# Optimization experiments

Hardware: AMD Instinct MI355X
Metric: run time of the kernel (lower is better)

## Reference

```python
import jax, jax.numpy as jnp
import numpy as np

NUM_HEADS = 16
HIDDEN = 1024
MASKED_BIAS = -10000.0


def setup_inputs() -> dict:
    key = jax.random.key(0)
    k1, k2 = jax.random.split(key)
    encodings = jax.random.normal(k1, (4, 2048, HIDDEN), dtype=jnp.float32)
    W_attn = jax.random.normal(k2, (HIDDEN, 3 * HIDDEN), dtype=jnp.float32) * (HIDDEN ** -0.5)
    b_attn = jnp.zeros((3 * HIDDEN,), dtype=jnp.float32)
    return {"encodings": encodings, "W_attn": W_attn, "b_attn": b_attn}


def reference(encodings, W_attn, b_attn):
    b, s, hidden = encodings.shape
    head_size = hidden // NUM_HEADS
    cattn = encodings @ W_attn + b_attn  # [b, s, 3*hidden]
    q, k, v = jnp.split(cattn, 3, axis=-1)
    # [b, s, hidden] -> [b, h, s, c]
    def split_heads(x):
        return x.reshape(b, s, NUM_HEADS, head_size).transpose(0, 2, 1, 3)
    q, k, v = split_heads(q), split_heads(k), split_heads(v)
    scores = jnp.einsum('bhfc,bhtc->bhft', q, k) / np.sqrt(head_size).astype(np.float32)
    causal = jnp.tril(jnp.ones((s, s), dtype=bool))[None, None]
    scores = jnp.where(causal, scores, jnp.float32(MASKED_BIAS))
    patterns = jax.nn.softmax(scores, axis=-1)
    ctx = jnp.einsum('bhft,bhtc->bhfc', patterns, v)
    # [b, h, s, c] -> [b, s, hidden]
    return ctx.transpose(0, 2, 1, 3).reshape(b, s, hidden)
```

## Files before the change

### kernel.cpp

```cpp
#include <hip/hip_runtime.h>

#define B_   4
#define S_   2048
#define HID  1024
#define NH   16
#define CH   64
#define M_   (B_ * S_)
#define N3   (3 * HID)
#define LDT2 72

typedef __attribute__((ext_vector_type(4))) float f32x4;
typedef __attribute__((ext_vector_type(8))) unsigned short u16x8;
typedef __attribute__((ext_vector_type(4))) unsigned short u16x4;

__device__ __forceinline__ unsigned short f2bf(float x) {
    unsigned u = __builtin_bit_cast(unsigned, x);
    u += 0x7fffu + ((u >> 16) & 1u);
    return (unsigned short)(u >> 16);
}
__device__ __forceinline__ float bf2f(unsigned short h) {
    unsigned u = ((unsigned)h) << 16;
    return __builtin_bit_cast(float, u);
}
__device__ __forceinline__ f32x4 mfma16(u16x8 a, u16x8 b, f32x4 c) {
    asm("v_mfma_f32_16x16x32_bf16 %0, %1, %2, %0" : "+v"(c) : "v"(a), "v"(b));
    return c;
}

__global__ __launch_bounds__(256) void k_split(const float* __restrict__ x,
                                               unsigned short* __restrict__ hi,
                                               unsigned short* __restrict__ lo,
                                               int n8) {
    int idx = blockIdx.x * 256 + threadIdx.x;
    if (idx >= n8) return;
    const f32x4* px = (const f32x4*)x + (size_t)idx * 2;
    f32x4 a = px[0], b = px[1];
    u16x8 h, l;
#pragma unroll
    for (int i = 0; i < 8; i++) {
        float xv = (i < 4) ? a[i] : b[i - 4];
        unsigned short hb = f2bf(xv);
        h[i] = hb;
        l[i] = f2bf(xv - bf2f(hb));
    }
    *(u16x8*)(hi + (size_t)idx * 8) = h;
    *(u16x8*)(lo + (size_t)idx * 8) = l;
}

__global__ __launch_bounds__(256) void k_tsplit(const float* __restrict__ W,
                                                unsigned short* __restrict__ WTh,
                                                unsigned short* __restrict__ WTl) {
    __shared__ float tile[32][33];
    int n0 = blockIdx.x * 32, k0 = blockIdx.y * 32;
    int tid = threadIdx.x;
    int r = tid >> 3, c0 = (tid & 7) * 4;
    f32x4 v = *(const f32x4*)(W + (size_t)(k0 + r) * N3 + n0 + c0);
#pragma unroll
    for (int i = 0; i < 4; i++) tile[r][c0 + i] = v[i];
    __syncthreads();
    u16x4 h, l;
#pragma unroll
    for (int i = 0; i < 4; i++) {
        float xv = tile[c0 + i][r];
        unsigned short hb = f2bf(xv);
        h[i] = hb;
        l[i] = f2bf(xv - bf2f(hb));
    }
    size_t o = (size_t)(n0 + r) * HID + k0 + c0;
    *(u16x4*)(WTh + o) = h;
    *(u16x4*)(WTl + o) = l;
}

__global__ __launch_bounds__(256, 2) void k_gemm(
    const unsigned short* __restrict__ Ah, const unsigned short* __restrict__ Al,
    const unsigned short* __restrict__ Bh, const unsigned short* __restrict__ Bl,
    const float* __restrict__ bias,
    unsigned short* __restrict__ Qh, unsigned short* __restrict__ Ql,
    unsigned short* __restrict__ Kh, unsigned short* __restrict__ Kl,
    unsigned short* __restrict__ Vt) {
    __shared__ __attribute__((aligned(16))) unsigned short sAh[128 * LDT2];
    __shared__ __attribute__((aligned(16))) unsigned short sAl[128 * LDT2];
    __shared__ __attribute__((aligned(16))) unsigned short sBh[128 * LDT2];
    __shared__ __attribute__((aligned(16))) unsigned short sBl[128 * LDT2];
    int tid = threadIdx.x;
    int m0 = blockIdx.y * 128, n0 = blockIdx.x * 128;
    int r = tid >> 1, kh2 = (tid & 1) * 32;
    int lane = tid & 63, w = tid >> 6;
    int wm = (w >> 1) * 64, wn = (w & 1) * 64;
    int l15 = lane & 15, l4 = lane >> 4;
    f32x4 acc[4][4] = {};
    size_t gA = (size_t)(m0 + r) * HID + kh2;
    size_t gB = (size_t)(n0 + r) * HID + kh2;

    u16x8 pf[4][4];
#pragma unroll
    for (int j = 0; j < 4; j++) {
        pf[0][j] = *(const u16x8*)(Ah + gA + j * 8);
        pf[1][j] = *(const u16x8*)(Al + gA + j * 8);
        pf[2][j] = *(const u16x8*)(Bh + gB + j * 8);
        pf[3][j] = *(const u16x8*)(Bl + gB + j * 8);
    }
#pragma unroll
    for (int j = 0; j < 4; j++) {
        *(u16x8*)&sAh[r * LDT2 + kh2 + j * 8] = pf[0][j];
        *(u16x8*)&sAl[r * LDT2 + kh2 + j * 8] = pf[1][j];
        *(u16x8*)&sBh[r * LDT2 + kh2 + j * 8] = pf[2][j];
        *(u16x8*)&sBl[r * LDT2 + kh2 + j * 8] = pf[3][j];
    }

    for (int k0 = 0; k0 < HID; k0 += 64) {
        __syncthreads();
        bool more = (k0 + 64 < HID);
        if (more) {
#pragma unroll
            for (int j = 0; j < 4; j++) {
                pf[0][j] = *(const u16x8*)(Ah + gA + k0 + 64 + j * 8);
                pf[1][j] = *(const u16x8*)(Al + gA + k0 + 64 + j * 8);
                pf[2][j] = *(const u16x8*)(Bh + gB + k0 + 64 + j * 8);
                pf[3][j] = *(const u16x8*)(Bl + gB + k0 + 64 + j * 8);
            }
        }
#pragma unroll
        for (int ks = 0; ks < 64; ks += 32) {
            u16x8 a0[4], a1[4], b0[4], b1[4];
#pragma unroll
            for (int i = 0; i < 4; i++) {
                int off = ks + l4 * 8;
                int row = wm + i * 16 + l15;
                a0[i] = *(const u16x8*)&sAh[row * LDT2 + off];
                a1[i] = *(const u16x8*)&sAl[row * LDT2 + off];
                int rowb = wn + i * 16 + l15;
                b0[i] = *(const u16x8*)&sBh[rowb * LDT2 + off];
                b1[i] = *(const u16x8*)&sBl[rowb * LDT2 + off];
            }
#pragma unroll
            for (int mt = 0; mt < 4; mt++)
#pragma unroll
                for (int nt = 0; nt < 4; nt++) {
                    acc[mt][nt] = mfma16(a0[mt], b0[nt], acc[mt][nt]);
                    acc[mt][nt] = mfma16(a0[mt], b1[nt], acc[mt][nt]);
                    acc[mt][nt] = mfma16(a1[mt], b0[nt], acc[mt][nt]);
                }
        }
        __syncthreads();
        if (more) {
#pragma unroll
            for (int j = 0; j < 4; j++) {
                *(u16x8*)&sAh[r * LDT2 + kh2 + j * 8] = pf[0][j];
                *(u16x8*)&sAl[r * LDT2 + kh2 + j * 8] = pf[1][j];
                *(u16x8*)&sBh[r * LDT2 + kh2 + j * 8] = pf[2][j];
                *(u16x8*)&sBl[r * LDT2 + kh2 + j * 8] = pf[3][j];
            }
        }
    }

#pragma unroll
    for (int mt = 0; mt < 4; mt++)
#pragma unroll
        for (int nt = 0; nt < 4; nt++) {
            int n = n0 + wn + nt * 16 + l15;
            float bv = bias[n];
            int which = n >> 10, hid = n & 1023;
            int h = hid >> 6, c = hid & 63;
            int mbase = m0 + wm + mt * 16 + l4 * 4;
            int b = mbase >> 11, sbase = mbase & 2047;
            int bh = b * NH + h;
            if (which == 2) {
                u16x4 pv;
#pragma unroll
                for (int jj = 0; jj < 4; jj++) pv[jj] = f2bf(acc[mt][nt][jj] + bv);
                *(u16x4*)(Vt + ((size_t)bh * CH + c) * S_ + sbase) = pv;
            } else {
                unsigned short* __restrict__ dh = (which == 0) ? Qh : Kh;
                unsigned short* __restrict__ dl = (which == 0) ? Ql : Kl;
                float sc = (which == 0) ? 0.125f : 1.0f;
#pragma unroll
                for (int jj = 0; jj < 4; jj++) {
                    float val = (acc[mt][nt][jj] + bv) * sc;
                    unsigned short hb = f2bf(val);
                    size_t so = ((size_t)bh * S_ + sbase + jj) * CH + c;
                    dh[so] = hb;
                    dl[so] = f2bf(val - bf2f(hb));
                }
            }
        }
}

__global__ __launch_bounds__(256, 2) void k_attn(const unsigned short* __restrict__ Qh,
                                                 const unsigned short* __restrict__ Ql,
                                                 const unsigned short* __restrict__ Kh,
                                                 const unsigned short* __restrict__ Kl,
                                                 const unsigned short* __restrict__ Vt,
                                                 float* __restrict__ out) {
    __shared__ __attribute__((aligned(16))) unsigned short sKh[128 * 64];
    __shared__ __attribute__((aligned(16))) unsigned short sKl[128 * 64];
    __shared__ __attribute__((aligned(16))) unsigned short sVT[64 * 128];
    __shared__ __attribute__((aligned(16))) unsigned short sP[4][32 * 128];
    int tid = threadIdx.x, lane = tid & 63, w = tid >> 6;
    int l15 = lane & 15, l4 = lane >> 4;
    int qt = gridDim.x - 1 - blockIdx.x;
    int bh = blockIdx.y;
    int b = bh >> 4, h = bh & 15;
    size_t head_off = (size_t)bh * S_ * CH;
    const unsigned short* Qhp = Qh + head_off;
    const unsigned short* Qlp = Ql + head_off;
    const unsigned short* Khp = Kh + head_off;
    const unsigned short* Klp = Kl + head_off;
    const unsigned short* Vtp = Vt + (size_t)bh * CH * S_;

    u16x8 qh[2][2], ql[2][2];
#pragma unroll
    for (int m = 0; m < 2; m++)
#pragma unroll
        for (int cc = 0; cc < 2; cc++) {
            size_t o = (size_t)(qt * 128 + w * 32 + m * 16 + l15) * CH + cc * 32 + l4 * 8;
            qh[m][cc] = *(const u16x8*)(Qhp + o);
            ql[m][cc] = *(const u16x8*)(Qlp + o);
        }

    f32x4 ctx[2][4] = {};
    float mrun[2][4], lrun[2][4];
#pragma unroll
    for (int m = 0; m < 2; m++)
#pragma unroll
        for (int j = 0; j < 4; j++) { mrun[m][j] = -1e30f; lrun[m][j] = 0.f; }

    for (int kt = 0; kt <= qt; kt++) {
        __syncthreads();
#pragma unroll
        for (int j = 0; j < 4; j++) {
            int idx = tid + j * 256;
            int rr = idx >> 3, slot = idx & 7;
            size_t g = (size_t)(kt * 128 + rr) * CH + slot * 8;
            int bo = (slot * 16) ^ ((rr & 7) << 4);
            *(u16x8*)((char*)sKh + rr * 128 + bo) = *(const u16x8*)(Khp + g);
            *(u16x8*)((char*)sKl + rr * 128 + bo) = *(const u16x8*)(Klp + g);
        }
#pragma unroll
        for (int j = 0; j < 4; j++) {
            int idx = tid + j * 256;
            int cc = idx >> 4, slot = idx & 15;
            size_t g = (size_t)cc * S_ + kt * 128 + slot * 8;
            int bo = (slot * 16) ^ ((cc & 7) << 4);
            *(u16x8*)((char*)sVT + cc * 256 + bo) = *(const u16x8*)(Vtp + g);
        }
        __syncthreads();

        f32x4 sa[2][8];
#pragma unroll
        for (int m = 0; m < 2; m++)
#pragma unroll
            for (int nt = 0; nt < 8; nt++) sa[m][nt] = f32x4{0.f, 0.f, 0.f, 0.f};
#pragma unroll
        for (int nt = 0; nt < 8; nt++) {
            int rowb = nt * 16 + l15;
            int swb = (rowb & 7) << 4;
            u16x8 kbh[2], kbl[2];
#pragma unroll
            for (int cc = 0; cc < 2; cc++) {
                int off = (cc * 64 + l4 * 16) ^ swb;
                kbh[cc] = *(const u16x8*)((char*)sKh + rowb * 128 + off);
                kbl[cc] = *(const u16x8*)((char*)sKl + rowb * 128 + off);
            }
#pragma unroll
            for (int m = 0; m < 2; m++)
#pragma unroll
                for (int cc = 0; cc < 2; cc++) {
                    sa[m][nt] = mfma16(qh[m][cc], kbh[cc], sa[m][nt]);
                    sa[m][nt] = mfma16(qh[m][cc], kbl[cc], sa[m][nt]);
                    sa[m][nt] = mfma16(ql[m][cc], kbh[cc], sa[m][nt]);
                }
        }
        if (kt == qt) {
#pragma unroll
            for (int m = 0; m < 2; m++)
#pragma unroll
                for (int nt = 0; nt < 8; nt++) {
                    int t = nt * 16 + l15;
#pragma unroll
                    for (int jj = 0; jj < 4; jj++) {
                        int f = w * 32 + m * 16 + l4 * 4 + jj;
                        if (t > f) sa[m][nt][jj] = -10000.0f;
                    }
                }
        }
#pragma unroll
        for (int m = 0; m < 2; m++)
#pragma unroll
            for (int jj = 0; jj < 4; jj++) {
                float rx = sa[m][0][jj];
#pragma unroll
                for (int nt = 1; nt < 8; nt++) rx = fmaxf(rx, sa[m][nt][jj]);
                rx = fmaxf(rx, __shfl_xor(rx, 1));
                rx = fmaxf(rx, __shfl_xor(rx, 2));
                rx = fmaxf(rx, __shfl_xor(rx, 4));
                rx = fmaxf(rx, __shfl_xor(rx, 8));
                float mnew = fmaxf(mrun[m][jj], rx);
                float sc = __expf(mrun[m][jj] - mnew);
                mrun[m][jj] = mnew;
                float ps = 0.f;
                int fm = m * 16 + l4 * 4 + jj;
                int swp = (fm & 7) << 4;
#pragma unroll
                for (int nt = 0; nt < 8; nt++) {
                    float p = __expf(sa[m][nt][jj] - mnew);
                    ps += p;
                    int bo = ((nt * 16 + l15) * 2) ^ swp;
                    *(unsigned short*)((char*)&sP[w][0] + fm * 256 + bo) = f2bf(p);
                }
                lrun[m][jj] = lrun[m][jj] * sc + ps;
#pragma unroll
                for (int nc = 0; nc < 4; nc++) ctx[m][nc][jj] *= sc;
            }
#pragma unroll
        for (int tk = 0; tk < 4; tk++) {
            u16x8 pa[2];
#pragma unroll
            for (int m = 0; m < 2; m++) {
                int row = m * 16 + l15;
                int off = (tk * 64 + l4 * 16) ^ ((row & 7) << 4);
                pa[m] = *(const u16x8*)((char*)&sP[w][0] + row * 256 + off);
            }
#pragma unroll
            for (int nc = 0; nc < 4; nc++) {
                int rowv = nc * 16 + l15;
                int off = (tk * 64 + l4 * 16) ^ ((rowv & 7) << 4);
                u16x8 vb = *(const u16x8*)((char*)sVT + rowv * 256 + off);
#pragma unroll
                for (int m = 0; m < 2; m++) ctx[m][nc] = mfma16(pa[m], vb, ctx[m][nc]);
            }
        }
    }
#pragma unroll
    for (int m = 0; m < 2; m++)
#pragma unroll
        for (int jj = 0; jj < 4; jj++) {
            float ls = lrun[m][jj];
            ls += __shfl_xor(ls, 1);
            ls += __shfl_xor(ls, 2);
            ls += __shfl_xor(ls, 4);
            ls += __shfl_xor(ls, 8);
            float inv = 1.0f / ls;
            int f = qt * 128 + w * 32 + m * 16 + l4 * 4 + jj;
#pragma unroll
            for (int nc = 0; nc < 4; nc++) {
                int c = nc * 16 + l15;
                out[((size_t)(b * S_ + f)) * HID + h * CH + c] = ctx[m][nc][jj] * inv;
            }
        }
}

extern "C" void kernel_launch(void* const* d_in, const int* in_sizes, int n_in,
                              void* d_out, int out_size, void* d_ws, size_t ws_size,
                              hipStream_t stream) {
    const float* enc  = (const float*)d_in[0];
    const float* W    = (const float*)d_in[1];
    const float* bias = (const float*)d_in[2];
    float* out = (float*)d_out;

    unsigned short* A_hi = (unsigned short*)d_ws;
    unsigned short* A_lo = A_hi + (size_t)M_ * HID;
    unsigned short* WTh  = A_lo + (size_t)M_ * HID;
    unsigned short* WTl  = WTh + (size_t)N3 * HID;
    unsigned short* Qh   = WTl + (size_t)N3 * HID;
    unsigned short* Ql   = Qh + (size_t)M_ * HID;
    unsigned short* Kh   = Ql + (size_t)M_ * HID;
    unsigned short* Kl   = Kh + (size_t)M_ * HID;
    unsigned short* Vt   = Kl + (size_t)M_ * HID;

    int n8 = (M_ * HID) / 8;
    k_split<<<dim3(n8 / 256), 256, 0, stream>>>(enc, A_hi, A_lo, n8);
    k_tsplit<<<dim3(N3 / 32, HID / 32), 256, 0, stream>>>(W, WTh, WTl);
    k_gemm<<<dim3(N3 / 128, M_ / 128), 256, 0, stream>>>(A_hi, A_lo, WTh, WTl, bias,
                                                         Qh, Ql, Kh, Kl, Vt);
    k_attn<<<dim3(S_ / 128, B_ * NH), 256, 0, stream>>>(Qh, Ql, Kh, Kl, Vt, out);
}
```

Before: 536.5 us.

## Pair causal query tiles per block and alias P buffer onto K smem

Each attention block now processes two query tiles (qt and NT-1-qt) so every block has equal causal work, and the grid is halved. The separate P scratch buffer is aliased onto the K shared-memory region, guarded by an extra barrier, which cuts LDS use so launch bounds can go from 2 to 3 blocks per CU. The change also adds s_setprio around the MFMA sections and widens the swizzle mask to 16 rows. The cost is an extra __syncthreads per key tile and tighter register limits, which may cause spills.

After: 685.9 us. 27.9% more time.

```diff
diff --git a/kernel.cpp b/kernel.cpp
--- a/kernel.cpp
+++ b/kernel.cpp
@@ -186,19 +186,19 @@
         }
 }
 
-__global__ __launch_bounds__(256, 2) void k_attn(const unsigned short* __restrict__ Qh,
+__global__ __launch_bounds__(256, 3) void k_attn(const unsigned short* __restrict__ Qh,
                                                  const unsigned short* __restrict__ Ql,
                                                  const unsigned short* __restrict__ Kh,
                                                  const unsigned short* __restrict__ Kl,
                                                  const unsigned short* __restrict__ Vt,
                                                  float* __restrict__ out) {
-    __shared__ __attribute__((aligned(16))) unsigned short sKh[128 * 64];
-    __shared__ __attribute__((aligned(16))) unsigned short sKl[128 * 64];
+    __shared__ __attribute__((aligned(16))) unsigned short sKbuf[2 * 128 * 64];
     __shared__ __attribute__((aligned(16))) unsigned short sVT[64 * 128];
-    __shared__ __attribute__((aligned(16))) unsigned short sP[4][32 * 128];
+    char* const sKhB = (char*)sKbuf;
+    char* const sKlB = (char*)sKbuf + 16384;
     int tid = threadIdx.x, lane = tid & 63, w = tid >> 6;
     int l15 = lane & 15, l4 = lane >> 4;
-    int qt = gridDim.x - 1 - blockIdx.x;
+    char* const sPB = (char*)sKbuf + w * 8192;
     int bh = blockIdx.y;
     int b = bh >> 4, h = bh & 15;
     size_t head_off = (size_t)bh * S_ * CH;
@@ -207,147 +207,159 @@
     const unsigned short* Khp = Kh + head_off;
     const unsigned short* Klp = Kl + head_off;
     const unsigned short* Vtp = Vt + (size_t)bh * CH * S_;
-
-    u16x8 qh[2][2], ql[2][2];
-#pragma unroll
-    for (int m = 0; m < 2; m++)
-#pragma unroll
-        for (int cc = 0; cc < 2; cc++) {
-            size_t o = (size_t)(qt * 128 + w * 32 + m * 16 + l15) * CH + cc * 32 + l4 * 8;
-            qh[m][cc] = *(const u16x8*)(Qhp + o);
-            ql[m][cc] = *(const u16x8*)(Qlp + o);
-        }
-
-    f32x4 ctx[2][4] = {};
-    float mrun[2][4], lrun[2][4];
-#pragma unroll
-    for (int m = 0; m < 2; m++)
-#pragma unroll
-        for (int j = 0; j < 4; j++) { mrun[m][j] = -1e30f; lrun[m][j] = 0.f; }
-
-    for (int kt = 0; kt <= qt; kt++) {
+    const int NT = S_ / 128;
+
+    for (int pass = 0; pass < 2; pass++) {
+        int qt = pass ? (NT - 1 - (int)blockIdx.x) : (int)blockIdx.x;
+
+        u16x8 qh[2][2], ql[2][2];
+#pragma unroll
+        for (int m = 0; m < 2; m++)
+#pragma unroll
+            for (int cc = 0; cc < 2; cc++) {
+                size_t o = (size_t)(qt * 128 + w * 32 + m * 16 + l15) * CH + cc * 32 + l4 * 8;
+                qh[m][cc] = *(const u16x8*)(Qhp + o);
+                ql[m][cc] = *(const u16x8*)(Qlp + o);
+            }
+
+        f32x4 ctx[2][4] = {};
+        float mrun[2][4], lrun[2][4];
+#pragma unroll
+        for (int m = 0; m < 2; m++)
+#pragma unroll
+            for (int j = 0; j < 4; j++) { mrun[m][j] = -1e30f; lrun[m][j] = 0.f; }
+
+        for (int kt = 0; kt <= qt; kt++) {
+            __syncthreads();
+#pragma unroll
+            for (int j = 0; j < 4; j++) {
+                int idx = tid + j * 256;
+                int rr = idx >> 3, slot = idx & 7;
+                size_t g = (size_t)(kt * 128 + rr) * CH + slot * 8;
+                int bo = (slot * 16) ^ ((rr & 7) << 4);
+                *(u16x8*)(sKhB + rr * 128 + bo) = *(const u16x8*)(Khp + g);
+                *(u16x8*)(sKlB + rr * 128 + bo) = *(const u16x8*)(Klp + g);
+            }
+#pragma unroll
+            for (int j = 0; j < 4; j++) {
+                int idx = tid + j * 256;
+                int cc = idx >> 4, slot = idx & 15;
+                size_t g = (size_t)cc * S_ + kt * 128 + slot * 8;
+                int bo = (slot * 16) ^ ((cc & 15) << 4);
+                *(u16x8*)((char*)sVT + cc * 256 + bo) = *(const u16x8*)(Vtp + g);
+            }
+            __syncthreads();
+
+            f32x4 sa[2][8];
+#pragma unroll
+            for (int m = 0; m < 2; m++)
+#pragma unroll
+                for (int nt = 0; nt < 8; nt++) sa[m][nt] = f32x4{0.f, 0.f, 0.f, 0.f};
+            __builtin_amdgcn_s_setprio(1);
+#pragma unroll
+            for (int nt = 0; nt < 8; nt++) {
+                int rowb = nt * 16 + l15;
+                int swb = (rowb & 7) << 4;
+                u16x8 kbh[2], kbl[2];
+#pragma unroll
+                for (int cc = 0; cc < 2; cc++) {
+                    int off = (cc * 64 + l4 * 16) ^ swb;
+                    kbh[cc] = *(const u16x8*)(sKhB + rowb * 128 + off);
+                    kbl[cc] = *(const u16x8*)(sKlB + rowb * 128 + off);
+                }
+#pragma unroll
+                for (int m = 0; m < 2; m++)
+#pragma unroll
+                    for (int cc = 0; cc < 2; cc++) {
+                        sa[m][nt] = mfma16(qh[m][cc], kbh[cc], sa[m][nt]);
+                        sa[m][nt] = mfma16(qh[m][cc], kbl[cc], sa[m][nt]);
+                        sa[m][nt] = mfma16(ql[m][cc], kbh[cc], sa[m][nt]);
+                    }
+            }
+            __builtin_amdgcn_s_setprio(0);
+            if (kt == qt) {
+#pragma unroll
+                for (int m = 0; m < 2; m++)
+#pragma unroll
+                    for (int nt = 0; nt < 8; nt++) {
+                        int t = nt * 16 + l15;
+#pragma unroll
+                        for (int jj = 0; jj < 4; jj++) {
+                            int f = w * 32 + m * 16 + l4 * 4 + jj;
+                            if (t > f) sa[m][nt][jj] = -10000.0f;
+                        }
+                    }
+            }
+            __syncthreads();
+
+#pragma unroll
+            for (int m = 0; m < 2; m++)
+#pragma unroll
+                for (int jj = 0; jj < 4; jj++) {
+                    float rx = sa[m][0][jj];
+#pragma unroll
+                    for (int nt = 1; nt < 8; nt++) rx = fmaxf(rx, sa[m][nt][jj]);
+                    rx = fmaxf(rx, __shfl_xor(rx, 1));
+                    rx = fmaxf(rx, __shfl_xor(rx, 2));
+                    rx = fmaxf(rx, __shfl_xor(rx, 4));
+                    rx = fmaxf(rx, __shfl_xor(rx, 8));
+                    float mnew = fmaxf(mrun[m][jj], rx);
+                    float sc = __expf(mrun[m][jj] - mnew);
+                    mrun[m][jj] = mnew;
+                    float ps = 0.f;
+                    int fm = m * 16 + l4 * 4 + jj;
+                    int swp = (fm & 15) << 4;
+#pragma unroll
+                    for (int nt = 0; nt < 8; nt++) {
+                        float p = __expf(sa[m][nt][jj] - mnew);
+                        ps += p;
+                        int bo = ((nt * 16 + l15) * 2) ^ swp;
+                        *(unsigned short*)(sPB + fm * 256 + bo) = f2bf(p);
+                    }
+                    lrun[m][jj] = lrun[m][jj] * sc + ps;
+#pragma unroll
+                    for (int nc = 0; nc < 4; nc++) ctx[m][nc][jj] *= sc;
+                }
+            __builtin_amdgcn_s_setprio(1);
+#pragma unroll
+            for (int tk = 0; tk < 4; tk++) {
+                u16x8 pa[2];
+#pragma unroll
+                for (int m = 0; m < 2; m++) {
+                    int row = m * 16 + l15;
+                    int off = (tk * 64 + l4 * 16) ^ ((row & 15) << 4);
+                    pa[m] = *(const u16x8*)(sPB + row * 256 + off);
+                }
+#pragma unroll
+                for (int nc = 0; nc < 4; nc++) {
+                    int rowv = nc * 16 + l15;
+                    int off = (tk * 64 + l4 * 16) ^ ((rowv & 15) << 4);
+                    u16x8 vb = *(const u16x8*)((char*)sVT + rowv * 256 + off);
+#pragma unroll
+                    for (int m = 0; m < 2; m++) ctx[m][nc] = mfma16(pa[m], vb, ctx[m][nc]);
+                }
+            }
+            __builtin_amdgcn_s_setprio(0);
+        }
+#pragma unroll
+        for (int m = 0; m < 2; m++)
+#pragma unroll
+            for (int jj = 0; jj < 4; jj++) {
+                float ls = lrun[m][jj];
+                ls += __shfl_xor(ls, 1);
+                ls += __shfl_xor(ls, 2);
+                ls += __shfl_xor(ls, 4);
+                ls += __shfl_xor(ls, 8);
+                float inv = 1.0f / ls;
+                int f = qt * 128 + w * 32 + m * 16 + l4 * 4 + jj;
+#pragma unroll
+                for (int nc = 0; nc < 4; nc++) {
+                    int c = nc * 16 + l15;
+                    out[((size_t)(b * S_ + f)) * HID + h * CH + c] = ctx[m][nc][jj] * inv;
+                }
+            }
         __syncthreads();
-#pragma unroll
-        for (int j = 0; j < 4; j++) {
-            int idx = tid + j * 256;
-            int rr = idx >> 3, slot = idx & 7;
-            size_t g = (size_t)(kt * 128 + rr) * CH + slot * 8;
-            int bo = (slot * 16) ^ ((rr & 7) << 4);
-            *(u16x8*)((char*)sKh + rr * 128 + bo) = *(const u16x8*)(Khp + g);
-            *(u16x8*)((char*)sKl + rr * 128 + bo) = *(const u16x8*)(Klp + g);
-        }
-#pragma unroll
-        for (int j = 0; j < 4; j++) {
-            int idx = tid + j * 256;
-            int cc = idx >> 4, slot = idx & 15;
-            size_t g = (size_t)cc * S_ + kt * 128 + slot * 8;
-            int bo = (slot * 16) ^ ((cc & 7) << 4);
-            *(u16x8*)((char*)sVT + cc * 256 + bo) = *(const u16x8*)(Vtp + g);
-        }
-        __syncthreads();
-
-        f32x4 sa[2][8];
-#pragma unroll
-        for (int m = 0; m < 2; m++)
-#pragma unroll
-            for (int nt = 0; nt < 8; nt++) sa[m][nt] = f32x4{0.f, 0.f, 0.f, 0.f};
-#pragma unroll
-        for (int nt = 0; nt < 8; nt++) {
-            int rowb = nt * 16 + l15;
-            int swb = (rowb & 7) << 4;
-            u16x8 kbh[2], kbl[2];
-#pragma unroll
-            for (int cc = 0; cc < 2; cc++) {
-                int off = (cc * 64 + l4 * 16) ^ swb;
-                kbh[cc] = *(const u16x8*)((char*)sKh + rowb * 128 + off);
-                kbl[cc] = *(const u16x8*)((char*)sKl + rowb * 128 + off);
-            }
-#pragma unroll
-            for (int m = 0; m < 2; m++)
-#pragma unroll
-                for (int cc = 0; cc < 2; cc++) {
-                    sa[m][nt] = mfma16(qh[m][cc], kbh[cc], sa[m][nt]);
-                    sa[m][nt] = mfma16(qh[m][cc], kbl[cc], sa[m][nt]);
-                    sa[m][nt] = mfma16(ql[m][cc], kbh[cc], sa[m][nt]);
-                }
-        }
-        if (kt == qt) {
-#pragma unroll
-            for (int m = 0; m < 2; m++)
-#pragma unroll
-                for (int nt = 0; nt < 8; nt++) {
-                    int t = nt * 16 + l15;
-#pragma unroll
-                    for (int jj = 0; jj < 4; jj++) {
-                        int f = w * 32 + m * 16 + l4 * 4 + jj;
-                        if (t > f) sa[m][nt][jj] = -10000.0f;
-                    }
-                }
-        }
-#pragma unroll
-        for (int m = 0; m < 2; m++)
-#pragma unroll
-            for (int jj = 0; jj < 4; jj++) {
-                float rx = sa[m][0][jj];
-#pragma unroll
-                for (int nt = 1; nt < 8; nt++) rx = fmaxf(rx, sa[m][nt][jj]);
-                rx = fmaxf(rx, __shfl_xor(rx, 1));
-                rx = fmaxf(rx, __shfl_xor(rx, 2));
-                rx = fmaxf(rx, __shfl_xor(rx, 4));
-                rx = fmaxf(rx, __shfl_xor(rx, 8));
-                float mnew = fmaxf(mrun[m][jj], rx);
-                float sc = __expf(mrun[m][jj] - mnew);
-                mrun[m][jj] = mnew;
-                float ps = 0.f;
-                int fm = m * 16 + l4 * 4 + jj;
-                int swp = (fm & 7) << 4;
-#pragma unroll
-                for (int nt = 0; nt < 8; nt++) {
-                    float p = __expf(sa[m][nt][jj] - mnew);
-                    ps += p;
-                    int bo = ((nt * 16 + l15) * 2) ^ swp;
-                    *(unsigned short*)((char*)&sP[w][0] + fm * 256 + bo) = f2bf(p);
-                }
-                lrun[m][jj] = lrun[m][jj] * sc + ps;
-#pragma unroll
-                for (int nc = 0; nc < 4; nc++) ctx[m][nc][jj] *= sc;
-            }
-#pragma unroll
-        for (int tk = 0; tk < 4; tk++) {
-            u16x8 pa[2];
-#pragma unroll
-            for (int m = 0; m < 2; m++) {
-                int row = m * 16 + l15;
-                int off = (tk * 64 + l4 * 16) ^ ((row & 7) << 4);
-                pa[m] = *(const u16x8*)((char*)&sP[w][0] + row * 256 + off);
-            }
-#pragma unroll
-            for (int nc = 0; nc < 4; nc++) {
-                int rowv = nc * 16 + l15;
-                int off = (tk * 64 + l4 * 16) ^ ((rowv & 7) << 4);
-                u16x8 vb = *(const u16x8*)((char*)sVT + rowv * 256 + off);
-#pragma unroll
-                for (int m = 0; m < 2; m++) ctx[m][nc] = mfma16(pa[m], vb, ctx[m][nc]);
-            }
-        }
-    }
-#pragma unroll
-    for (int m = 0; m < 2; m++)
-#pragma unroll
-        for (int jj = 0; jj < 4; jj++) {
-            float ls = lrun[m][jj];
-            ls += __shfl_xor(ls, 1);
-            ls += __shfl_xor(ls, 2);
-            ls += __shfl_xor(ls, 4);
-            ls += __shfl_xor(ls, 8);
-            float inv = 1.0f / ls;
-            int f = qt * 128 + w * 32 + m * 16 + l4 * 4 + jj;
-#pragma unroll
-            for (int nc = 0; nc < 4; nc++) {
-                int c = nc * 16 + l15;
-                out[((size_t)(b * S_ + f)) * HID + h * CH + c] = ctx[m][nc][jj] * inv;
-            }
-        }
+    }
 }
 
 extern "C" void kernel_launch(void* const* d_in, const int* in_sizes, int n_in,
@@ -373,5 +385,5 @@
     k_tsplit<<<dim3(N3 / 32, HID / 32), 256, 0, stream>>>(W, WTh, WTl);
     k_gemm<<<dim3(N3 / 128, M_ / 128), 256, 0, stream>>>(A_hi, A_lo, WTh, WTl, bias,
                                                          Qh, Ql, Kh, Kl, Vt);
-    k_attn<<<dim3(S_ / 128, B_ * NH), 256, 0, stream>>>(Qh, Ql, Kh, Kl, Vt, out);
-}
+    k_attn<<<dim3(S_ / 128 / 2, B_ * NH), 256, 0, stream>>>(Qh, Ql, Kh, Kl, Vt, out);
+}
```
